# Kernel optimization log

Hardware: AMD Instinct MI355X
Metric: run time of the kernel (lower is better)

## Reference

```python
import jax, jax.numpy as jnp
import numpy as np

B, D, E, H = 8192, 2048, 8, 128

def setup_inputs() -> dict:
    key = jax.random.key(0)
    ks = jax.random.split(key, 9)
    s_d = 1.0 / np.sqrt(D)
    s_h = 1.0 / np.sqrt(H)
    return {
        "x": jax.random.normal(ks[0], (B, D), dtype=jnp.float32),
        "gate_w": jax.random.normal(ks[1], (D, E), dtype=jnp.float32) * s_d,
        "gate_b": jnp.zeros((E,), dtype=jnp.float32),
        "W1": jax.random.normal(ks[2], (E, D, H), dtype=jnp.float32) * s_d,
        "b1": jnp.zeros((E, H), dtype=jnp.float32),
        "W2": jax.random.normal(ks[3], (E, H, H), dtype=jnp.float32) * s_h,
        "b2": jnp.zeros((E, H), dtype=jnp.float32),
        "W3": jax.random.normal(ks[4], (E, H, D), dtype=jnp.float32) * s_h,
        "b3": jnp.zeros((E, D), dtype=jnp.float32),
    }

def reference(x, gate_w, gate_b, W1, b1, W2, b2, W3, b3):
    # Adaptive gate: softmax over experts
    gates = jax.nn.softmax(x @ gate_w + gate_b, axis=1)          # [B, E]
    # All experts as one batched (grouped) GEMM over the expert axis.
    h1 = jax.nn.silu(jnp.einsum('bd,edh->ebh', x, W1) + b1[:, None, :])   # [E, B, H]
    h2 = jax.nn.silu(jnp.einsum('ebh,ehk->ebk', h1, W2) + b2[:, None, :]) # [E, B, H]
    y = jnp.einsum('ebh,ehd->ebd', h2, W3) + b3[:, None, :]               # [E, B, D]
    # Gate-weighted sum over experts (fused reduction, no [B,E,D] stack kept)
    out = jnp.einsum('be,ebd->bd', gates, y)                     # [B, D]
    return out
```

## Files before the change

### kernel.cpp

```cpp
#include <hip/hip_runtime.h>


typedef __attribute__((ext_vector_type(8))) short short8;
typedef __attribute__((ext_vector_type(4))) float f32x4;

#define B_SZ 8192
#define D_SZ 2048
#define E_SZ 8
#define H_SZ 128

__device__ __forceinline__ short f2bf(float f) {
  unsigned u = __builtin_bit_cast(unsigned, f);
  unsigned r = (u + 0x7fffu + ((u >> 16) & 1u)) >> 16;
  return (short)r;
}

__device__ __forceinline__ float silu_f(float v) {
  return v / (1.f + __expf(-v));
}

__device__ __forceinline__ void gload_lds16(const void* g, void* l) {
  __builtin_amdgcn_global_load_lds(
      (const __attribute__((address_space(1))) void*)g,
      (__attribute__((address_space(3))) void*)l,
      16, 0, 0);
}

template<int NHT>
__device__ __forceinline__ void core128(const short* __restrict__ A,
                                        const short* __restrict__ B,
                                        short* lds, f32x4 acc[4][4])
{
  const int tid  = threadIdx.x;
  const int lane = tid & 63;
  const int wid  = tid >> 6;
  const int wr = wid >> 1, wc = wid & 1;
  const int lm = lane & 15, lk = lane >> 4;
  const int wl = (tid & ~63) * 8;

  auto STAGE = [&](int eta) {
    const size_t go = (size_t)(eta >> 1)*8192 + (size_t)(eta & 1)*4096;
    short* l = lds + (eta & 1)*8192;
    gload_lds16(A + go + tid*8,        l + wl);
    gload_lds16(A + go + 2048 + tid*8, l + 2048 + wl);
    gload_lds16(B + go + tid*8,        l + 4096 + wl);
    gload_lds16(B + go + 2048 + tid*8, l + 6144 + wl);
  };

  STAGE(0);
  __syncthreads();
  for (int eta = 0; eta < NHT; ++eta) {
    if (eta + 1 < NHT) STAGE(eta + 1);
    const short* la = lds + (eta & 1)*8192 + lk*1024 + (wr*64 + lm)*8;
    const short* lb = lds + (eta & 1)*8192 + 4096 + lk*1024 + (wc*64 + lm)*8;
    short8 av[4], bv[4];
    #pragma unroll
    for (int f = 0; f < 4; ++f) av[f] = *(const short8*)(la + f*128);
    #pragma unroll
    for (int f = 0; f < 4; ++f) bv[f] = *(const short8*)(lb + f*128);
    #pragma unroll
    for (int i = 0; i < 4; ++i)
      #pragma unroll
      for (int j = 0; j < 4; ++j)
        acc[i][j] = __builtin_amdgcn_mfma_f32_16x16x32_bf16(av[i], bv[j], acc[i][j], 0, 0, 0);
    __syncthreads();
  }
}

__global__ __launch_bounds__(256)
void k_cvt_gate(const float* __restrict__ x,  const float* __restrict__ W1,
                const float* __restrict__ W2, const float* __restrict__ W3,
                const float* __restrict__ gw, const float* __restrict__ gb,
                short* __restrict__ xf, short* __restrict__ w1f,
                short* __restrict__ w2f, short* __restrict__ w3f,
                float* __restrict__ gates)
{
  if (blockIdx.x < 10304) {
    const int gi = blockIdx.x * 256 + threadIdx.x;
    if (gi < 2097152) {
      const int t = gi >> 10, r = gi & 1023;
      const int bt = t >> 5, kt = t & 31;
      const int kg = r >> 7, p = r & 127;
      const float* src = x + (size_t)(bt*128 + p)*2048 + kt*64 + kg*8;
      const float4 v0 = *(const float4*)src;
      const float4 v1 = *(const float4*)(src + 4);
      short8 o;
      o[0]=f2bf(v0.x); o[1]=f2bf(v0.y); o[2]=f2bf(v0.z); o[3]=f2bf(v0.w);
      o[4]=f2bf(v1.x); o[5]=f2bf(v1.y); o[6]=f2bf(v1.z); o[7]=f2bf(v1.w);
      *(short8*)(xf + (size_t)gi*8) = o;
    } else if (gi < 2097152 + 262144) {
      const int g = gi - 2097152;
      const int t = g >> 10, r = g & 1023;
      const int e = t >> 5, kt = t & 31;
      const int kg = r >> 7, p = r & 127;
      const int k0 = kt*64 + kg*8;
      short8 o;
      #pragma unroll
      for (int j = 0; j < 8; ++j)
        o[j] = f2bf(W1[(size_t)e*262144 + (size_t)(k0 + j)*128 + p]);
      *(short8*)(w1f + (size_t)g*8) = o;
    } else if (gi < 2097152 + 262144 + 16384) {
      const int g = gi - (2097152 + 262144);
      const int t = g >> 10, r = g & 1023;
      const int e = t >> 1, kt = t & 1;
      const int kg = r >> 7, p = r & 127;
      const int k0 = kt*64 + kg*8;
      short8 o;
      #pragma unroll
      for (int j = 0; j < 8; ++j)
        o[j] = f2bf(W2[(size_t)e*16384 + (size_t)(k0 + j)*128 + p]);
      *(short8*)(w2f + (size_t)g*8) = o;
    } else if (gi < 2637824) {
      const int g = gi - 2375680;
      const int t = g >> 10, r = g & 1023;
      const int nt = t >> 4, kt = t & 15;
      const int kg = r >> 7, p = r & 127;
      const int k0 = kt*64 + kg*8;
      short8 o;
      #pragma unroll
      for (int j = 0; j < 8; ++j) {
        const int k = k0 + j;
        o[j] = f2bf(W3[(size_t)(k >> 7)*262144 + (size_t)(k & 127)*2048 + nt*128 + p]);
      }
      *(short8*)(w3f + (size_t)g*8) = o;
    }
  } else {
    const int wid = threadIdx.x >> 6, lane = threadIdx.x & 63;
    const int row = (blockIdx.x - 10304) * 4 + wid;
    const float* xr = x + (size_t)row * 2048;
    float acc[8] = {0.f,0.f,0.f,0.f,0.f,0.f,0.f,0.f};
    for (int it = 0; it < 32; ++it) {
      const int k = it*64 + lane;
      const float xv = xr[k];
      const float4 g0 = *(const float4*)(gw + (size_t)k*8);
      const float4 g1 = *(const float4*)(gw + (size_t)k*8 + 4);
      acc[0] += xv*g0.x; acc[1] += xv*g0.y; acc[2] += xv*g0.z; acc[3] += xv*g0.w;
      acc[4] += xv*g1.x; acc[5] += xv*g1.y; acc[6] += xv*g1.z; acc[7] += xv*g1.w;
    }
    #pragma unroll
    for (int e = 0; e < 8; ++e) {
      #pragma unroll
      for (int d = 1; d < 64; d <<= 1)
        acc[e] += __shfl_xor(acc[e], d, 64);
    }
    if (lane == 0) {
      float lg[8], mx = -1e30f;
      #pragma unroll
      for (int e = 0; e < 8; ++e) { lg[e] = acc[e] + gb[e]; mx = fmaxf(mx, lg[e]); }
      float s = 0.f;
      #pragma unroll
      for (int e = 0; e < 8; ++e) { lg[e] = __expf(lg[e] - mx); s += lg[e]; }
      const float inv = 1.f / s;
      #pragma unroll
      for (int e = 0; e < 8; ++e) gates[(size_t)row*8 + e] = lg[e] * inv;
    }
  }
}

__global__ __launch_bounds__(256, 2)
void k_gemm12f(const short* __restrict__ xf, const short* __restrict__ w1f,
               const short* __restrict__ w2f,
               const float* __restrict__ b1, const float* __restrict__ b2,
               const float* __restrict__ gates, short* __restrict__ h2gf)
{
  __shared__ short lds[16384];
  const int b = blockIdx.x;
  const int xcd = b & 7, idx = b >> 3;
  const int bt = xcd*8 + (idx & 7);
  const int e  = idx >> 3;

  f32x4 acc[4][4] = {};
  core128<64>(xf  + (size_t)bt*32*8192,
              w1f + (size_t)e*32*8192,
              lds, acc);

  const int tid = threadIdx.x, lane = tid & 63, wid = tid >> 6;
  const int wr = wid >> 1, wc = wid & 1;
  const int lm = lane & 15, lk = lane >> 4, lr = lane >> 4;

  short8 bvAll[2][2][4];
  #pragma unroll
  for (int kt = 0; kt < 2; ++kt)
  #pragma unroll
  for (int ks = 0; ks < 2; ++ks)
  #pragma unroll
  for (int fn = 0; fn < 4; ++fn)
    bvAll[kt][ks][fn] = *(const short8*)(
        w2f + (size_t)e*16384 + kt*8192 + (ks*4 + lk)*1024
            + (wc*64 + fn*16 + lm)*8);

  float gv[4][4];
  #pragma unroll
  for (int fm = 0; fm < 4; ++fm)
  #pragma unroll
  for (int i = 0; i < 4; ++i)
    gv[fm][i] = gates[(size_t)(bt*128 + wr*64 + fm*16 + lr*4 + i)*8 + e];

  float b1v[4];
  #pragma unroll
  for (int fn = 0; fn < 4; ++fn) b1v[fn] = b1[e*H_SZ + wc*64 + fn*16 + lm];
  #pragma unroll
  for (int fm = 0; fm < 4; ++fm)
  #pragma unroll
  for (int i = 0; i < 4; ++i) {
    const int m = wr*64 + fm*16 + lr*4 + i;
    #pragma unroll
    for (int fn = 0; fn < 4; ++fn) {
      const int n = wc*64 + fn*16 + lm;
      const float v = silu_f(acc[fm][fn][i] + b1v[fn]);
      lds[(n >> 3)*1024 + m*8 + (n & 7)] = f2bf(v);
    }
  }
  __syncthreads();

  f32x4 acc2[4][4] = {};
  #pragma unroll
  for (int kt = 0; kt < 2; ++kt)
  #pragma unroll
  for (int ks = 0; ks < 2; ++ks) {
    short8 av[4];
    #pragma unroll
    for (int f = 0; f < 4; ++f)
      av[f] = *(const short8*)(lds + (kt*8 + ks*4 + lk)*1024 + (wr*64 + f*16 + lm)*8);
    #pragma unroll
    for (int i = 0; i < 4; ++i)
      #pragma unroll
      for (int j = 0; j < 4; ++j)
        acc2[i][j] = __builtin_amdgcn_mfma_f32_16x16x32_bf16(
            av[i], bvAll[kt][ks][j], acc2[i][j], 0, 0, 0);
  }
  __syncthreads();

  float b2v[4];
  #pragma unroll
  for (int fn = 0; fn < 4; ++fn) b2v[fn] = b2[e*H_SZ + wc*64 + fn*16 + lm];
  #pragma unroll
  for (int fm = 0; fm < 4; ++fm)
  #pragma unroll
  for (int i = 0; i < 4; ++i) {
    const int m = wr*64 + fm*16 + lr*4 + i;
    const float g = gv[fm][i];
    #pragma unroll
    for (int fn = 0; fn < 4; ++fn) {
      const int n = wc*64 + fn*16 + lm;
      const float v = silu_f(acc2[fm][fn][i] + b2v[fn]) * g;
      lds[(n >> 3)*1024 + m*8 + (n & 7)] = f2bf(v);
    }
  }
  __syncthreads();

  #pragma unroll
  for (int q = 0; q < 8; ++q) {
    const int li = q*2048 + tid*8;
    const int t2 = li >> 13, off = li & 8191;
    *(short8*)(h2gf + ((size_t)bt*16 + e*2 + t2)*8192 + off) =
        *(const short8*)(lds + li);
  }
}

__global__ __launch_bounds__(256, 4)
void k_gemm3(const short* __restrict__ h2gf, const short* __restrict__ w3f,
             const float* __restrict__ b3, const float* __restrict__ gates,
             float* __restrict__ out)
{
  __shared__ short lds[16384];
  const int b = blockIdx.x;
  const int xcd = b & 7, idx = b >> 3;
  const int bt = xcd*8 + (idx & 7);
  const int nt = idx >> 3;

  f32x4 acc[4][4] = {};
  core128<32>(h2gf + (size_t)bt*16*8192,
              w3f  + (size_t)nt*16*8192,
              lds, acc);

  const int tid = threadIdx.x, lane = tid & 63, wid = tid >> 6;
  const int wr = wid >> 1, wc = wid & 1, lm = lane & 15, lr = lane >> 4;
  float b3c[4][8];
  #pragma unroll
  for (int fn = 0; fn < 4; ++fn) {
    const int n = nt*128 + wc*64 + fn*16 + lm;
    #pragma unroll
    for (int e = 0; e < 8; ++e) b3c[fn][e] = b3[(size_t)e*D_SZ + n];
  }
  #pragma unroll
  for (int fm = 0; fm < 4; ++fm)
  #pragma unroll
  for (int i = 0; i < 4; ++i) {
    const int m = bt*128 + wr*64 + fm*16 + lr*4 + i;
    const float4 ga  = *(const float4*)(gates + (size_t)m*8);
    const float4 gbv = *(const float4*)(gates + (size_t)m*8 + 4);
    #pragma unroll
    for (int fn = 0; fn < 4; ++fn) {
      const int n = nt*128 + wc*64 + fn*16 + lm;
      const float bias = ga.x*b3c[fn][0] + ga.y*b3c[fn][1] + ga.z*b3c[fn][2] + ga.w*b3c[fn][3]
                       + gbv.x*b3c[fn][4] + gbv.y*b3c[fn][5] + gbv.z*b3c[fn][6] + gbv.w*b3c[fn][7];
      out[(size_t)m*D_SZ + n] = acc[fm][fn][i] + bias;
    }
  }
}

extern "C" void kernel_launch(void* const* d_in, const int* in_sizes, int n_in,
                              void* d_out, int out_size, void* d_ws, size_t ws_size,
                              hipStream_t stream)
{
  (void)in_sizes; (void)n_in; (void)out_size; (void)ws_size;
  const float* x  = (const float*)d_in[0];
  const float* gw = (const float*)d_in[1];
  const float* gb = (const float*)d_in[2];
  const float* W1 = (const float*)d_in[3];
  const float* b1 = (const float*)d_in[4];
  const float* W2 = (const float*)d_in[5];
  const float* b2 = (const float*)d_in[6];
  const float* W3 = (const float*)d_in[7];
  const float* b3 = (const float*)d_in[8];
  float* out = (float*)d_out;

  char* ws = (char*)d_ws;
  short* xf    = (short*)ws;  ws += (size_t)B_SZ*D_SZ*2;
  short* w1f   = (short*)ws;  ws += (size_t)E_SZ*D_SZ*H_SZ*2;
  short* w2f   = (short*)ws;  ws += (size_t)E_SZ*H_SZ*H_SZ*2;
  short* w3f   = (short*)ws;  ws += (size_t)E_SZ*H_SZ*D_SZ*2;
  float* gates = (float*)ws;  ws += (size_t)B_SZ*E_SZ*4;
  short* h2gf  = (short*)ws;  ws += (size_t)B_SZ*E_SZ*H_SZ*2;

  k_cvt_gate<<<dim3(12352), dim3(256), 0, stream>>>(x, W1, W2, W3, gw, gb,
                                                    xf, w1f, w2f, w3f, gates);
  k_gemm12f <<<dim3(512),  dim3(256), 0, stream>>>(xf, w1f, w2f, b1, b2, gates, h2gf);
  k_gemm3   <<<dim3(1024), dim3(256), 0, stream>>>(h2gf, w3f, b3, gates, out);
}
```

Baseline: 147.2 us.

## Transpose x conversion through LDS and batch gate rows per wave

The x fp32-to-bf16 conversion now loads row-contiguous float4 chunks of each 128x64 tile into swizzled shared memory, then writes the tiled layout with contiguous 16-byte stores. The goal is fully coalesced global reads and writes. The gate softmax computation now handles four rows per wave with vectorized loads, reusing gate weight loads across rows and cutting the gate block count. The cost is shared memory use and an extra barrier in the conversion blocks.

```diff
diff --git a/kernel.cpp b/kernel.cpp
--- a/kernel.cpp
+++ b/kernel.cpp
@@ -2,6 +2,7 @@
 
 
 typedef __attribute__((ext_vector_type(8))) short short8;
+typedef __attribute__((ext_vector_type(4))) short bf16x4;
 typedef __attribute__((ext_vector_type(4))) float f32x4;
 
 #define B_SZ 8192
@@ -75,20 +76,84 @@
                 short* __restrict__ w2f, short* __restrict__ w3f,
                 float* __restrict__ gates)
 {
-  if (blockIdx.x < 10304) {
-    const int gi = blockIdx.x * 256 + threadIdx.x;
-    if (gi < 2097152) {
-      const int t = gi >> 10, r = gi & 1023;
-      const int bt = t >> 5, kt = t & 31;
-      const int kg = r >> 7, p = r & 127;
-      const float* src = x + (size_t)(bt*128 + p)*2048 + kt*64 + kg*8;
-      const float4 v0 = *(const float4*)src;
-      const float4 v1 = *(const float4*)(src + 4);
-      short8 o;
-      o[0]=f2bf(v0.x); o[1]=f2bf(v0.y); o[2]=f2bf(v0.z); o[3]=f2bf(v0.w);
-      o[4]=f2bf(v1.x); o[5]=f2bf(v1.y); o[6]=f2bf(v1.z); o[7]=f2bf(v1.w);
-      *(short8*)(xf + (size_t)gi*8) = o;
-    } else if (gi < 2097152 + 262144) {
+  __shared__ short lt[8192];
+  const int b = blockIdx.x;
+  const int tid = threadIdx.x;
+
+  if (b < 512) {
+    const int lane = tid & 63, wid = tid >> 6;
+    const int row0 = b*16 + wid*4;
+    float acc[4][8] = {};
+    #pragma unroll
+    for (int it = 0; it < 8; ++it) {
+      const int k = it*256 + lane*4;
+      float4 xv[4];
+      #pragma unroll
+      for (int r = 0; r < 4; ++r)
+        xv[r] = *(const float4*)(x + (size_t)(row0 + r)*2048 + k);
+      float4 gv[4][2];
+      #pragma unroll
+      for (int d = 0; d < 4; ++d) {
+        gv[d][0] = *(const float4*)(gw + (size_t)(k + d)*8);
+        gv[d][1] = *(const float4*)(gw + (size_t)(k + d)*8 + 4);
+      }
+      #pragma unroll
+      for (int r = 0; r < 4; ++r) {
+        const float xr[4] = {xv[r].x, xv[r].y, xv[r].z, xv[r].w};
+        #pragma unroll
+        for (int d = 0; d < 4; ++d) {
+          acc[r][0] += xr[d]*gv[d][0].x; acc[r][1] += xr[d]*gv[d][0].y;
+          acc[r][2] += xr[d]*gv[d][0].z; acc[r][3] += xr[d]*gv[d][0].w;
+          acc[r][4] += xr[d]*gv[d][1].x; acc[r][5] += xr[d]*gv[d][1].y;
+          acc[r][6] += xr[d]*gv[d][1].z; acc[r][7] += xr[d]*gv[d][1].w;
+        }
+      }
+    }
+    #pragma unroll
+    for (int r = 0; r < 4; ++r)
+      #pragma unroll
+      for (int e = 0; e < 8; ++e)
+        #pragma unroll
+        for (int d = 1; d < 64; d <<= 1)
+          acc[r][e] += __shfl_xor(acc[r][e], d, 64);
+    if (lane < 4) {
+      float lg[8], mx = -1e30f;
+      #pragma unroll
+      for (int e = 0; e < 8; ++e) { lg[e] = acc[lane][e] + gb[e]; mx = fmaxf(mx, lg[e]); }
+      float s = 0.f;
+      #pragma unroll
+      for (int e = 0; e < 8; ++e) { lg[e] = __expf(lg[e] - mx); s += lg[e]; }
+      const float inv = 1.f / s;
+      #pragma unroll
+      for (int e = 0; e < 8; ++e) gates[(size_t)(row0 + lane)*8 + e] = lg[e] * inv;
+    }
+  } else if (b < 2560) {
+    const int t = b - 512;
+    const int bt = t >> 5, kt = t & 31;
+    const float* xb = x + (size_t)bt*128*2048 + kt*64;
+    #pragma unroll
+    for (int u = 0; u < 8; ++u) {
+      const int flat = u*1024 + tid*4;
+      const int row = flat >> 6, kk = flat & 63;
+      const float4 v = *(const float4*)(xb + (size_t)row*2048 + kk);
+      const int kg = kk >> 3;
+      bf16x4 o;
+      o[0] = f2bf(v.x); o[1] = f2bf(v.y); o[2] = f2bf(v.z); o[3] = f2bf(v.w);
+      const int s = (kg*1024 + row*8 + (kk & 7)) ^ ((kg & 7) << 3);
+      *(bf16x4*)(lt + s) = o;
+    }
+    __syncthreads();
+    short* dst = xf + (size_t)t*8192;
+    #pragma unroll
+    for (int u = 0; u < 4; ++u) {
+      const int li = u*2048 + tid*8;
+      const int kg = li >> 10;
+      const int s = li ^ ((kg & 7) << 3);
+      *(short8*)(dst + li) = *(const short8*)(lt + s);
+    }
+  } else {
+    const int gi = (b - 2560)*256 + tid + 2097152;
+    if (gi < 2097152 + 262144) {
       const int g = gi - 2097152;
       const int t = g >> 10, r = g & 1023;
       const int e = t >> 5, kt = t & 31;
@@ -123,36 +188,6 @@
         o[j] = f2bf(W3[(size_t)(k >> 7)*262144 + (size_t)(k & 127)*2048 + nt*128 + p]);
       }
       *(short8*)(w3f + (size_t)g*8) = o;
-    }
-  } else {
-    const int wid = threadIdx.x >> 6, lane = threadIdx.x & 63;
-    const int row = (blockIdx.x - 10304) * 4 + wid;
-    const float* xr = x + (size_t)row * 2048;
-    float acc[8] = {0.f,0.f,0.f,0.f,0.f,0.f,0.f,0.f};
-    for (int it = 0; it < 32; ++it) {
-      const int k = it*64 + lane;
-      const float xv = xr[k];
-      const float4 g0 = *(const float4*)(gw + (size_t)k*8);
-      const float4 g1 = *(const float4*)(gw + (size_t)k*8 + 4);
-      acc[0] += xv*g0.x; acc[1] += xv*g0.y; acc[2] += xv*g0.z; acc[3] += xv*g0.w;
-      acc[4] += xv*g1.x; acc[5] += xv*g1.y; acc[6] += xv*g1.z; acc[7] += xv*g1.w;
-    }
-    #pragma unroll
-    for (int e = 0; e < 8; ++e) {
-      #pragma unroll
-      for (int d = 1; d < 64; d <<= 1)
-        acc[e] += __shfl_xor(acc[e], d, 64);
-    }
-    if (lane == 0) {
-      float lg[8], mx = -1e30f;
-      #pragma unroll
-      for (int e = 0; e < 8; ++e) { lg[e] = acc[e] + gb[e]; mx = fmaxf(mx, lg[e]); }
-      float s = 0.f;
-      #pragma unroll
-      for (int e = 0; e < 8; ++e) { lg[e] = __expf(lg[e] - mx); s += lg[e]; }
-      const float inv = 1.f / s;
-      #pragma unroll
-      for (int e = 0; e < 8; ++e) gates[(size_t)row*8 + e] = lg[e] * inv;
     }
   }
 }
@@ -324,8 +359,8 @@
   float* gates = (float*)ws;  ws += (size_t)B_SZ*E_SZ*4;
   short* h2gf  = (short*)ws;  ws += (size_t)B_SZ*E_SZ*H_SZ*2;
 
-  k_cvt_gate<<<dim3(12352), dim3(256), 0, stream>>>(x, W1, W2, W3, gw, gb,
-                                                    xf, w1f, w2f, w3f, gates);
+  k_cvt_gate<<<dim3(4672), dim3(256), 0, stream>>>(x, W1, W2, W3, gw, gb,
+                                                   xf, w1f, w2f, w3f, gates);
   k_gemm12f <<<dim3(512),  dim3(256), 0, stream>>>(xf, w1f, w2f, b1, b2, gates, h2gf);
   k_gemm3   <<<dim3(1024), dim3(256), 0, stream>>>(h2gf, w3f, b3, gates, out);
 }
```

After: 135.7 us. 1.08x faster.
